# Performance work log

Hardware: AMD Instinct MI355X
Metric: run time of the kernel (lower is better)

Reference implementation:

```python
import jax, jax.numpy as jnp
import numpy as np
import math

B, S, E, H, DFF = 4, 1024, 1024, 16, 4096
HD = E // H
EPS = 1e-8


def setup_inputs() -> dict:
    key = jax.random.key(0)
    ks = jax.random.split(key, 16)
    sc = 0.02
    inp = {
        'x': jax.random.normal(ks[0], (B, S, E), jnp.float32),
        'mask': jax.random.randint(ks[1], (B, S, S), 0, 2, jnp.int32),
        'Wq': jax.random.normal(ks[2], (E, E), jnp.float32) * sc,
        'bq': jnp.zeros((E,), jnp.float32),
        'Wk': jax.random.normal(ks[3], (E, E), jnp.float32) * sc,
        'bk': jnp.zeros((E,), jnp.float32),
        'Wv': jax.random.normal(ks[4], (E, E), jnp.float32) * sc,
        'bv': jnp.zeros((E,), jnp.float32),
        'Wo': jax.random.normal(ks[5], (E, E), jnp.float32) * sc,
        'bo': jnp.zeros((E,), jnp.float32),
        'W1': jax.random.normal(ks[6], (DFF, E), jnp.float32) * sc,
        'b1': jnp.zeros((DFF,), jnp.float32),
        'W2': jax.random.normal(ks[7], (E, DFF), jnp.float32) * sc,
        'b2': jnp.zeros((E,), jnp.float32),
        'g1': jnp.ones((E,), jnp.float32),
        'be1': jnp.zeros((E,), jnp.float32),
        'g2': jnp.ones((E,), jnp.float32),
        'be2': jnp.zeros((E,), jnp.float32),
    }
    return inp


def _layernorm(x, g, b):
    # torch LayerNorm here: (x-mean)/(std+eps), std is unbiased (ddof=1)
    mean = jnp.mean(x, axis=-1, keepdims=True)
    std = jnp.std(x, axis=-1, keepdims=True, ddof=1)
    return g * (x - mean) / (std + EPS) + b


def _gelu(x):
    c = math.sqrt(2.0 / math.pi)
    return 0.5 * x * (1.0 + jnp.tanh(c * (x + 0.044715 * x ** 3)))


def _block(x, mask_f, Wq, bq, Wk, bk, Wv, bv, Wo, bo, W1, b1, W2, b2, g1, be1, g2, be2):
    # --- attention sublayer (pre-norm, residual) ---
    nx = _layernorm(x, g1, be1)
    q = (nx @ Wq.T + bq).reshape(B, S, H, HD).transpose(0, 2, 1, 3)  # [B,H,S,D]
    k = (nx @ Wk.T + bk).reshape(B, S, H, HD).transpose(0, 2, 1, 3)
    v = (nx @ Wv.T + bv).reshape(B, S, H, HD).transpose(0, 2, 1, 3)
    scores = jnp.einsum('bhqd,bhkd->bhqk', q, k) / math.sqrt(HD)
    m = mask_f[:, None, :, :]  # [B,1,S,S]
    scores = jnp.where(m == 0, jnp.float32(-0.01), scores * m)
    p = jax.nn.softmax(scores, axis=-1)
    o = jnp.einsum('bhqk,bhkd->bhqd', p, v)  # [B,H,S,D]
    o = o.transpose(0, 2, 1, 3).reshape(B, S, E)
    x = x + (o @ Wo.T + bo)
    # --- FFN sublayer ---
    nx2 = _layernorm(x, g2, be2)
    ff = _gelu(nx2 @ W1.T + b1) @ W2.T + b2
    return x + ff


def reference(x, mask, Wq, bq, Wk, bk, Wv, bv, Wo, bo, W1, b1, W2, b2, g1, be1, g2, be2):
    mask_f = mask.astype(jnp.float32)
    return _block(x, mask_f, Wq, bq, Wk, bk, Wv, bv, Wo, bo, W1, b1, W2, b2, g1, be1, g2, be2)
```

## Files before the change

kernel.cpp:

```cpp
#include <hip/hip_runtime.h>
#include <math.h>

typedef __attribute__((ext_vector_type(8))) short short8;
typedef __attribute__((ext_vector_type(4))) float f32x4;
typedef __attribute__((ext_vector_type(4))) int   i32x4v;

#define B_   4
#define S_   1024
#define E_   1024
#define H_   16
#define DFF_ 4096

#define HB_MAX 4.0f

__device__ __forceinline__ ushort f2bf(float f){
  unsigned int x = __float_as_uint(f);
  x += 0x7fffu + ((x >> 16) & 1u);
  return (ushort)(x >> 16);
}

__device__ __forceinline__ unsigned int pk_bf16_trunc(float a, float b){
  return __builtin_amdgcn_perm(__float_as_uint(b), __float_as_uint(a), 0x07060302u);
}

__device__ __forceinline__ float gelu_f(float x){
  const float c = 0.7978845608028654f;
  float u = 2.0f * c * (x + 0.044715f * x * x * x);
  return x / (1.0f + __expf(-u));
}

__device__ __forceinline__ void gl2lds16(const void* g, void* l){
  __builtin_amdgcn_global_load_lds(
      (const __attribute__((address_space(1))) void*)g,
      (__attribute__((address_space(3))) void*)l, 16, 0, 0);
}

__device__ __forceinline__ int q8(float x, float s){
  float v = fmaxf(fminf(x * s, 127.f), -127.f);
  return ((int)__builtin_rintf(v)) & 255;
}
__device__ __forceinline__ int pk_i8x4(float a, float b, float c, float d, float s){
  return q8(a,s) | (q8(b,s) << 8) | (q8(c,s) << 16) | (q8(d,s) << 24);
}

__global__ __launch_bounds__(256) void prep_kernel(
    const float* __restrict__ Wq, const float* __restrict__ Wk,
    const float* __restrict__ Wv, const float* __restrict__ Wo,
    const float* __restrict__ W1, const float* __restrict__ W2,
    const float* __restrict__ bq, const float* __restrict__ bk,
    const float* __restrict__ bv, const int* __restrict__ mask,
    unsigned char* __restrict__ bQKV8, float* __restrict__ sQKV,
    unsigned char* __restrict__ bWo8, float* __restrict__ sWo,
    unsigned char* __restrict__ bW18, float* __restrict__ sW1,
    unsigned char* __restrict__ bW28, float* __restrict__ sW2,
    float* __restrict__ cbias, unsigned long long* __restrict__ maskp)
{
  int blk = blockIdx.x, t = threadIdx.x;
  int w = t >> 6, ln = t & 63;

  if (blk < 2048){
    int row = blk * 4 + w;
    const float* src; unsigned char* dst; float* sdst;
    if (row < 1024){      src = Wq + (size_t)row * 1024;
                          dst = bQKV8 + (size_t)row * 1024; sdst = sQKV + row; }
    else if (row < 2048){ src = Wk + (size_t)(row - 1024) * 1024;
                          dst = bQKV8 + (size_t)row * 1024; sdst = sQKV + row; }
    else if (row < 3072){ src = Wv + (size_t)(row - 2048) * 1024;
                          dst = bQKV8 + (size_t)row * 1024; sdst = sQKV + row; }
    else if (row < 4096){ int r = row - 3072; src = Wo + (size_t)r * 1024;
                          dst = bWo8 + (size_t)r * 1024; sdst = sWo + r; }
    else                { int r = row - 4096; src = W1 + (size_t)r * 1024;
                          dst = bW18 + (size_t)r * 1024; sdst = sW1 + r; }
    float4 v[4]; float m = 0.f;
    #pragma unroll
    for (int i = 0; i < 4; i++){
      v[i] = ((const float4*)src)[ln + i * 64];
      m = fmaxf(m, fmaxf(fmaxf(fabsf(v[i].x), fabsf(v[i].y)),
                         fmaxf(fabsf(v[i].z), fabsf(v[i].w))));
    }
    #pragma unroll
    for (int o = 32; o; o >>= 1) m = fmaxf(m, __shfl_xor(m, o));
    float mx = m + 1e-20f, qs = 127.0f / mx;
    #pragma unroll
    for (int i = 0; i < 4; i++)
      ((int*)dst)[ln + i * 64] = pk_i8x4(v[i].x, v[i].y, v[i].z, v[i].w, qs);
    if (ln == 0) *sdst = mx * (1.0f / 127.0f);
    return;
  }
  if (blk < 2304){
    int r = (blk - 2048) * 4 + w;
    const float* src = W2 + (size_t)r * 4096;
    float4 v[16]; float m = 0.f;
    #pragma unroll
    for (int i = 0; i < 16; i++){
      v[i] = ((const float4*)src)[ln + i * 64];
      m = fmaxf(m, fmaxf(fmaxf(fabsf(v[i].x), fabsf(v[i].y)),
                         fmaxf(fabsf(v[i].z), fabsf(v[i].w))));
    }
    #pragma unroll
    for (int o = 32; o; o >>= 1) m = fmaxf(m, __shfl_xor(m, o));
    float mx = m + 1e-20f, qs = 127.0f / mx;
    #pragma unroll
    for (int i = 0; i < 16; i++)
      ((int*)(bW28 + (size_t)r * 4096))[ln + i * 64] =
          pk_i8x4(v[i].x, v[i].y, v[i].z, v[i].w, qs);
    if (ln == 0) sW2[r] = mx * (1.0f / 127.0f);
    return;
  }
  if (blk == 2304){
    #pragma unroll
    for (int r = 0; r < 12; r++){
      int idx = r * 256 + t;
      cbias[idx] = (idx < 1024) ? bq[idx] : (idx < 2048 ? bk[idx - 1024] : bv[idx - 2048]);
    }
    return;
  }
  int wbase = (blk - 2305) * 16 + w * 4;
  #pragma unroll
  for (int j = 0; j < 4; j++){
    int widx = wbase + j;
    int mv = mask[(size_t)widx * 64 + ln];
    unsigned long long bal = __ballot(mv != 0);
    if (ln == 0) maskp[widx] = bal;
  }
}

__global__ __launch_bounds__(256) void ln_i8(const float* __restrict__ x,
    const float* __restrict__ g, const float* __restrict__ be,
    unsigned char* __restrict__ out8, float* __restrict__ sOut){
  int row = blockIdx.x, t = threadIdx.x;
  float4 v = ((const float4*)(x + (size_t)row * E_))[t];
  float s = v.x + v.y + v.z + v.w;
  float q = v.x*v.x + v.y*v.y + v.z*v.z + v.w*v.w;
  #pragma unroll
  for (int o = 32; o; o >>= 1){ s += __shfl_xor(s, o); q += __shfl_xor(q, o); }
  __shared__ float ss[4], sq[4], sm[4];
  int w = t >> 6;
  if ((t & 63) == 0){ ss[w] = s; sq[w] = q; }
  __syncthreads();
  s = ss[0] + ss[1] + ss[2] + ss[3];
  q = sq[0] + sq[1] + sq[2] + sq[3];
  float mean = s * (1.0f / E_);
  float var  = fmaxf((q - (float)E_ * mean * mean) * (1.0f / (E_ - 1)), 0.0f);
  float inv = 1.0f / (sqrtf(var) + 1e-8f);
  float4 gv = ((const float4*)g)[t];
  float4 bv = ((const float4*)be)[t];
  float n0 = gv.x * (v.x - mean) * inv + bv.x;
  float n1 = gv.y * (v.y - mean) * inv + bv.y;
  float n2 = gv.z * (v.z - mean) * inv + bv.z;
  float n3 = gv.w * (v.w - mean) * inv + bv.w;
  float m = fmaxf(fmaxf(fabsf(n0), fabsf(n1)), fmaxf(fabsf(n2), fabsf(n3)));
  #pragma unroll
  for (int o = 32; o; o >>= 1) m = fmaxf(m, __shfl_xor(m, o));
  if ((t & 63) == 0) sm[w] = m;
  __syncthreads();
  float mx = fmaxf(fmaxf(sm[0], sm[1]), fmaxf(sm[2], sm[3])) + 1e-20f;
  float qs = 127.0f / mx;
  ((int*)(out8 + (size_t)row * E_))[t] = pk_i8x4(n0, n1, n2, n3, qs);
  if (t == 0) sOut[row] = mx * (1.0f / 127.0f);
}

__global__ __launch_bounds__(256) void ln2_fuse(const float* __restrict__ x,
    const float* __restrict__ P, const float* __restrict__ bo,
    const float* __restrict__ g, const float* __restrict__ be,
    float* __restrict__ x2, unsigned char* __restrict__ nx28, float* __restrict__ sOut){
  int row = blockIdx.x, t = threadIdx.x;
  size_t idx = (size_t)row * 256 + t;
  float4 v  = ((const float4*)x)[idx];
  float4 p0 = ((const float4*)P)[idx];
  float4 p1 = ((const float4*)P)[idx + 1048576];
  float4 bv0 = ((const float4*)bo)[t];
  v.x += p0.x + p1.x + bv0.x;
  v.y += p0.y + p1.y + bv0.y;
  v.z += p0.z + p1.z + bv0.z;
  v.w += p0.w + p1.w + bv0.w;
  ((float4*)x2)[idx] = v;
  float s = v.x + v.y + v.z + v.w;
  float q = v.x*v.x + v.y*v.y + v.z*v.z + v.w*v.w;
  #pragma unroll
  for (int o = 32; o; o >>= 1){ s += __shfl_xor(s, o); q += __shfl_xor(q, o); }
  __shared__ float ss[4], sq[4], sm[4];
  int w = t >> 6;
  if ((t & 63) == 0){ ss[w] = s; sq[w] = q; }
  __syncthreads();
  s = ss[0] + ss[1] + ss[2] + ss[3];
  q = sq[0] + sq[1] + sq[2] + sq[3];
  float mean = s * (1.0f / E_);
  float var  = fmaxf((q - (float)E_ * mean * mean) * (1.0f / (E_ - 1)), 0.0f);
  float inv = 1.0f / (sqrtf(var) + 1e-8f);
  float4 gv = ((const float4*)g)[t];
  float4 bev = ((const float4*)be)[t];
  float n0 = gv.x * (v.x - mean) * inv + bev.x;
  float n1 = gv.y * (v.y - mean) * inv + bev.y;
  float n2 = gv.z * (v.z - mean) * inv + bev.z;
  float n3 = gv.w * (v.w - mean) * inv + bev.w;
  float m = fmaxf(fmaxf(fabsf(n0), fabsf(n1)), fmaxf(fabsf(n2), fabsf(n3)));
  #pragma unroll
  for (int o = 32; o; o >>= 1) m = fmaxf(m, __shfl_xor(m, o));
  if ((t & 63) == 0) sm[w] = m;
  __syncthreads();
  float mx = fmaxf(fmaxf(sm[0], sm[1]), fmaxf(sm[2], sm[3])) + 1e-20f;
  float qs = 127.0f / mx;
  ((int*)(nx28 + (size_t)row * E_))[t] = pk_i8x4(n0, n1, n2, n3, qs);
  if (t == 0) sOut[row] = mx * (1.0f / 127.0f);
}

__global__ __launch_bounds__(256) void reduce_out(const float* __restrict__ x2,
    const float* __restrict__ P, const float* __restrict__ b2, float* __restrict__ out){
  size_t i = (size_t)blockIdx.x * 256 + threadIdx.x;
  int col4 = i & 255;
  float4 v  = ((const float4*)x2)[i];
  float4 p0 = ((const float4*)P)[i];
  float4 p1 = ((const float4*)P)[i + 1048576];
  float4 bv = ((const float4*)b2)[col4];
  float4 o;
  o.x = v.x + p0.x + p1.x + bv.x;
  o.y = v.y + p0.y + p1.y + bv.y;
  o.z = v.z + p0.z + p1.z + bv.z;
  o.w = v.w + p0.w + p1.w + bv.w;
  ((float4*)out)[i] = o;
}

template<int MODE>
__global__ __launch_bounds__(512) void gemm256_i8(
    const unsigned char* __restrict__ A8, const unsigned char* __restrict__ B8,
    const float* __restrict__ sA, const float* __restrict__ sB,
    const float* __restrict__ bias,
    ushort* __restrict__ Cb, unsigned char* __restrict__ C8, float* __restrict__ Pf,
    int K, int ldc)
{
  __shared__ __align__(16) unsigned char smem[2][2][32768];
  const int t = threadIdx.x, w = t >> 6, ln = t & 63;
  const int quad = ln >> 4, lc = ln & 15;
  const int wm = w >> 2, wn = w & 3;

  const int gx = gridDim.x;
  const int nwg = gx * gridDim.y;
  int f = blockIdx.y * gx + blockIdx.x;
  f = (f & 7) * (nwg >> 3) + (f >> 3);
  const int n0 = (f % gx) * 256;
  const int m0 = (f / gx) * 256;

  int kbeg = 0, nT = K >> 7;
  if (MODE == 2){
    int kh = K >> 1;
    kbeg = blockIdx.z * kh;
    nT = kh >> 7;
    Pf += (size_t)blockIdx.z * (4096 * 1024);
  }

  auto stage_half = [&](const unsigned char* g, unsigned char* l){
    #pragma unroll
    for (int rr = 0; rr < 2; rr++){
      int chunk = rr * 512 + t;
      int row = chunk >> 3;
      int co = ((chunk & 7) ^ (row & 7)) * 16;
      gl2lds16(g + (size_t)row * K + co, l + (size_t)(rr * 512 + (t & 448)) * 16);
    }
  };

  const unsigned char* gA = A8 + (size_t)m0 * K + kbeg;
  const unsigned char* gB = B8 + (size_t)n0 * K + kbeg;

  i32x4v acc[8][4];
  #pragma unroll
  for (int i = 0; i < 8; i++)
    #pragma unroll
    for (int j = 0; j < 4; j++) acc[i][j] = i32x4v{0, 0, 0, 0};

  stage_half(gA,                    &smem[0][0][0]);
  stage_half(gA + (size_t)128 * K,  &smem[0][0][0] + 16384);
  stage_half(gB,                    &smem[0][1][0]);
  stage_half(gB + (size_t)128 * K,  &smem[0][1][0] + 16384);
  asm volatile("s_waitcnt vmcnt(0)" ::: "memory");
  __builtin_amdgcn_s_barrier();
  asm volatile("" ::: "memory");

  for (int tk = 0; tk < nT; tk++){
    const int c = tk & 1;
    const unsigned char* Ab = &smem[c][0][0];
    const unsigned char* Bb = &smem[c][1][0];
    unsigned char* As1 = &smem[c ^ 1][0][0];
    unsigned char* Bs1 = &smem[c ^ 1][1][0];
    const bool pre = (tk + 1 < nT);
    const unsigned char* gAn = gA + (size_t)(tk + 1) * 128;
    const unsigned char* gBn = gB + (size_t)(tk + 1) * 128;

    #pragma unroll
    for (int p = 0; p < 4; p++){
      const int mh = p >> 1, nh = p & 1;
      if (p == 0 && pre){
        stage_half(gAn,                   As1);
        stage_half(gAn + (size_t)128 * K, As1 + 16384);
      }
      if (p == 1 && pre){
        stage_half(gBn,                   Bs1);
        stage_half(gBn + (size_t)128 * K, Bs1 + 16384);
      }
      i32x4v af[4][2], bfr[2][2];
      #pragma unroll
      for (int i = 0; i < 4; i++){
        int row = wm * 128 + (mh * 4 + i) * 16 + lc;
        int sw = row & 7;
        af[i][0] = *(const i32x4v*)(Ab + (size_t)row * 128 + (((0 + quad) ^ sw) * 16));
        af[i][1] = *(const i32x4v*)(Ab + (size_t)row * 128 + (((4 + quad) ^ sw) * 16));
      }
      #pragma unroll
      for (int j = 0; j < 2; j++){
        int row = wn * 64 + (nh * 2 + j) * 16 + lc;
        int sw = row & 7;
        bfr[j][0] = *(const i32x4v*)(Bb + (size_t)row * 128 + (((0 + quad) ^ sw) * 16));
        bfr[j][1] = *(const i32x4v*)(Bb + (size_t)row * 128 + (((4 + quad) ^ sw) * 16));
      }
      __builtin_amdgcn_s_barrier();
      asm volatile("s_waitcnt lgkmcnt(0)" ::: "memory");
      __builtin_amdgcn_s_setprio(1);
      #pragma unroll
      for (int kk2 = 0; kk2 < 2; kk2++)
        #pragma unroll
        for (int i = 0; i < 4; i++)
          #pragma unroll
          for (int j = 0; j < 2; j++)
            acc[mh * 4 + i][nh * 2 + j] = __builtin_amdgcn_mfma_i32_16x16x64_i8(
                af[i][kk2], bfr[j][kk2], acc[mh * 4 + i][nh * 2 + j], 0, 0, 0);
      __builtin_amdgcn_s_setprio(0);
      if (p == 3){
        asm volatile("s_waitcnt vmcnt(0)" ::: "memory");
      }
      __builtin_amdgcn_s_barrier();
      if (p == 3) asm volatile("" ::: "memory");
    }
  }

  if (MODE == 2){
    #pragma unroll
    for (int j = 0; j < 4; j++){
      int col = n0 + wn * 64 + j * 16 + lc;
      float sb = sB[col] * (HB_MAX / 127.0f);
      #pragma unroll
      for (int i = 0; i < 8; i++){
        int row0 = m0 + wm * 128 + i * 16 + quad * 4;
        #pragma unroll
        for (int r = 0; r < 4; r++)
          Pf[(size_t)(row0 + r) * 1024 + col] = (float)acc[i][j][r] * sb;
      }
    }
  } else {
    float sbv[4], bcv[4], scv[4];
    int colv[4];
    #pragma unroll
    for (int j = 0; j < 4; j++){
      int col = n0 + wn * 64 + j * 16 + lc;
      colv[j] = col;
      sbv[j] = sB[col];
      bcv[j] = bias[col];
      scv[j] = (MODE == 0 && col < 1024) ? 0.125f : 1.0f;
    }
    #pragma unroll
    for (int i = 0; i < 8; i++){
      #pragma unroll
      for (int r = 0; r < 4; r++){
        int row = m0 + wm * 128 + i * 16 + quad * 4 + r;
        float sa = sA[row];
        #pragma unroll
        for (int j = 0; j < 4; j++){
          float v = (float)acc[i][j][r] * sa * sbv[j] + bcv[j];
          if (MODE == 0){
            Cb[(size_t)row * ldc + colv[j]] = f2bf(v * scv[j]);
          } else {
            C8[(size_t)row * 4096 + colv[j]] =
                (unsigned char)q8(gelu_f(v), 127.0f / HB_MAX);
          }
        }
      }
    }
  }
}

__global__ __launch_bounds__(256) void vT_kernel(const ushort* __restrict__ QKV,
                                                 ushort* __restrict__ Vt){
  __shared__ ushort tile[64][68];
  int st = blockIdx.x;
  int bh = blockIdx.y;
  int b = bh >> 4, h = bh & 15;
  int t = threadIdx.x;
  #pragma unroll
  for (int it = 0; it < 4; it++){
    int idx = it * 256 + t;
    int r = idx >> 4, c4 = (idx & 15) * 4;
    ushort4 v = *(const ushort4*)(QKV + ((size_t)(b*1024 + st*64 + r)) * 3072 + 2048 + h*64 + c4);
    *(ushort4*)(&tile[r][c4]) = v;
  }
  __syncthreads();
  #pragma unroll
  for (int it = 0; it < 4; it++){
    int idx = it * 256 + t;
    int d = idx >> 4, s4 = (idx & 15) * 4;
    ushort4 o;
    o.x = tile[s4+0][d]; o.y = tile[s4+1][d]; o.z = tile[s4+2][d]; o.w = tile[s4+3][d];
    *(ushort4*)(Vt + ((size_t)bh * 64 + d) * 1024 + st*64 + s4) = o;
  }
}

__global__ __launch_bounds__(256) void attn_kernel(
    const ushort* __restrict__ QKV, const ushort* __restrict__ Vt,
    const unsigned long long* __restrict__ maskp, unsigned char* __restrict__ O8)
{
  __shared__ __align__(16) ushort Ks[2][64 * 64];
  __shared__ __align__(16) ushort Vs[2][64 * 64];
  __shared__ __align__(16) ushort Ps[4][16 * 72];

  const int t = threadIdx.x, w = t >> 6, ln = t & 63;
  const int quad = ln >> 4, lc = ln & 15;
  const int bh = blockIdx.x, b = bh >> 4;
  const int q0 = blockIdx.y * 64;
  const int coff = (bh & 15) * 64;
  const size_t rb = (size_t)b * S_;

  const int myq = q0 + w*16 + lc;
  const ushort* qrow = QKV + (rb + myq) * 3072 + coff;
  short8 qf0 = *(const short8*)(qrow + quad*8);
  short8 qf1 = *(const short8*)(qrow + 32 + quad*8);
  const unsigned long long* mrow = maskp + (rb + myq) * 16;

  auto stage = [&](int kt, int buf){
    int k0 = kt * 64;
    #pragma unroll
    for (int it = 0; it < 2; it++){
      int chunk = it * 256 + t;
      int row = chunk >> 3;
      int co = ((chunk & 7) ^ (row & 7)) * 8;
      gl2lds16(QKV + (rb + k0 + row) * 3072 + 1024 + coff + co,
               Ks[buf] + (size_t)(it*256 + (t & 192)) * 8);
      gl2lds16(Vt + ((size_t)bh * 64 + row) * 1024 + k0 + co,
               Vs[buf] + (size_t)(it*256 + (t & 192)) * 8);
    }
  };

  f32x4 of[4];
  #pragma unroll
  for (int gd = 0; gd < 4; gd++) of[gd] = f32x4{0.f, 0.f, 0.f, 0.f};
  float lsum = 0.0f;
  const float PM = 0.99004983f;

  stage(0, 0);
  for (int kt = 0; kt < 16; kt++){
    int buf = kt & 1;
    unsigned long long m64 = mrow[kt];
    __syncthreads();
    if (kt < 15) stage(kt + 1, buf ^ 1);
    const ushort* ks = Ks[buf];
    const ushort* vs = Vs[buf];

    f32x4 sf[4];
    #pragma unroll
    for (int g = 0; g < 4; g++){
      int krow = g*16 + lc;
      short8 kf0 = *(const short8*)(ks + krow*64 + ((quad       ^ (lc & 7)) * 8));
      short8 kf1 = *(const short8*)(ks + krow*64 + (((4 + quad) ^ (lc & 7)) * 8));
      f32x4 z = f32x4{0.f, 0.f, 0.f, 0.f};
      z = __builtin_amdgcn_mfma_f32_16x16x32_bf16(kf0, qf0, z, 0, 0, 0);
      z = __builtin_amdgcn_mfma_f32_16x16x32_bf16(kf1, qf1, z, 0, 0, 0);
      sf[g] = z;
    }

    #pragma unroll
    for (int g = 0; g < 4; g++){
      unsigned int b4 = (unsigned int)(m64 >> (g*16 + quad*4)) & 0xFu;
      float p0 = (b4 & 1u) ? __expf(sf[g][0]) : PM;
      float p1 = (b4 & 2u) ? __expf(sf[g][1]) : PM;
      float p2 = (b4 & 4u) ? __expf(sf[g][2]) : PM;
      float p3 = (b4 & 8u) ? __expf(sf[g][3]) : PM;
      lsum += p0 + p1 + p2 + p3;
      uint2 pw;
      pw.x = pk_bf16_trunc(p0, p1);
      pw.y = pk_bf16_trunc(p2, p3);
      *(uint2*)(&Ps[w][lc*72 + g*16 + quad*4]) = pw;
    }

    short8 pf0 = *(const short8*)(&Ps[w][lc*72 + quad*8]);
    short8 pf1 = *(const short8*)(&Ps[w][lc*72 + 32 + quad*8]);
    #pragma unroll
    for (int gd = 0; gd < 4; gd++){
      int vrow = gd*16 + lc;
      short8 vf0 = *(const short8*)(vs + vrow*64 + ((quad       ^ (lc & 7)) * 8));
      short8 vf1 = *(const short8*)(vs + vrow*64 + (((4 + quad) ^ (lc & 7)) * 8));
      of[gd] = __builtin_amdgcn_mfma_f32_16x16x32_bf16(vf0, pf0, of[gd], 0, 0, 0);
      of[gd] = __builtin_amdgcn_mfma_f32_16x16x32_bf16(vf1, pf1, of[gd], 0, 0, 0);
    }
  }

  lsum += __shfl_xor(lsum, 16);
  lsum += __shfl_xor(lsum, 32);
  float inv = 1.0f / lsum;

  unsigned char* orow = O8 + (rb + myq) * E_ + coff;
  #pragma unroll
  for (int gd = 0; gd < 4; gd++){
    int pk = pk_i8x4(of[gd][0] * inv, of[gd][1] * inv,
                     of[gd][2] * inv, of[gd][3] * inv, 127.0f / HB_MAX);
    *(int*)(orow + gd*16 + quad*4) = pk;
  }
}

extern "C" void kernel_launch(void* const* d_in, const int* in_sizes, int n_in,
                              void* d_out, int out_size, void* d_ws, size_t ws_size,
                              hipStream_t stream)
{
  const float* x   = (const float*)d_in[0];
  const int*   mask= (const int*)  d_in[1];
  const float* Wq  = (const float*)d_in[2];
  const float* bq  = (const float*)d_in[3];
  const float* Wk  = (const float*)d_in[4];
  const float* bk  = (const float*)d_in[5];
  const float* Wv  = (const float*)d_in[6];
  const float* bv  = (const float*)d_in[7];
  const float* Wo  = (const float*)d_in[8];
  const float* bo  = (const float*)d_in[9];
  const float* W1  = (const float*)d_in[10];
  const float* b1  = (const float*)d_in[11];
  const float* W2  = (const float*)d_in[12];
  const float* b2  = (const float*)d_in[13];
  const float* g1  = (const float*)d_in[14];
  const float* be1 = (const float*)d_in[15];
  const float* g2  = (const float*)d_in[16];
  const float* be2 = (const float*)d_in[17];
  float* out = (float*)d_out;

  char* ws = (char*)d_ws;
  size_t off = 0;
  auto alloc = [&](size_t bytes) -> void* {
    void* p = ws + off; off += (bytes + 255) & ~(size_t)255; return p;
  };
  const size_t MM = 1024 * 1024;
  unsigned char* bQKV8 = (unsigned char*)alloc(3 * MM);
  float* sQKV  = (float*)alloc(3072 * 4);
  unsigned char* bWo8 = (unsigned char*)alloc(MM);
  float* sWo   = (float*)alloc(1024 * 4);
  unsigned char* bW18 = (unsigned char*)alloc(4 * MM);
  float* sW1   = (float*)alloc(4096 * 4);
  unsigned char* bW28 = (unsigned char*)alloc(4 * MM);
  float* sW2   = (float*)alloc(1024 * 4);
  float* cbias = (float*)alloc(3072 * 4);
  unsigned long long* maskp = (unsigned long long*)alloc(65536 * 8);
  unsigned char* nx8  = (unsigned char*)alloc(4 * MM);
  float* sX1   = (float*)alloc(4096 * 4);
  ushort* QKV  = (ushort*)alloc(12 * MM * 2);
  ushort* VtG  = (ushort*)alloc(4 * MM * 2);
  unsigned char* Ob8 = (unsigned char*)alloc(4 * MM);
  float*  x2   = (float*) alloc(4 * MM * 4);
  unsigned char* nx28 = (unsigned char*)alloc(4 * MM);
  float* sX2   = (float*)alloc(4096 * 4);
  unsigned char* hb8  = (unsigned char*)alloc(16 * MM);

  float* Pbuf = (float*)nx8;

  prep_kernel<<<6401, 256, 0, stream>>>(Wq, Wk, Wv, Wo, W1, W2, bq, bk, bv, mask,
                                        bQKV8, sQKV, bWo8, sWo, bW18, sW1, bW28, sW2,
                                        cbias, maskp);

  ln_i8<<<4096, 256, 0, stream>>>(x, g1, be1, nx8, sX1);

  gemm256_i8<0><<<dim3(12, 16), 512, 0, stream>>>(
      nx8, bQKV8, sX1, sQKV, cbias, QKV, nullptr, nullptr, 1024, 3072);

  vT_kernel<<<dim3(16, 64), 256, 0, stream>>>(QKV, VtG);

  attn_kernel<<<dim3(64, 16), 256, 0, stream>>>(QKV, VtG, maskp, Ob8);

  gemm256_i8<2><<<dim3(4, 16, 2), 512, 0, stream>>>(
      Ob8, bWo8, nullptr, sWo, nullptr, nullptr, nullptr, Pbuf, 1024, 1024);

  ln2_fuse<<<4096, 256, 0, stream>>>(x, Pbuf, bo, g2, be2, x2, nx28, sX2);

  gemm256_i8<1><<<dim3(16, 16), 512, 0, stream>>>(
      nx28, bW18, sX2, sW1, b1, nullptr, hb8, nullptr, 1024, 4096);

  gemm256_i8<2><<<dim3(4, 16, 2), 512, 0, stream>>>(
      hb8, bW28, nullptr, sW2, nullptr, nullptr, nullptr, Pbuf, 4096, 1024);

  reduce_out<<<4096, 256, 0, stream>>>(x2, Pbuf, b2, out);
}
```

Measured before the change: 329.8 us.

## Add BN template to int8 GEMM, widen attention blocks, use exp2 softmax

The int8 GEMM gains a BN template parameter so the split-K Wo and W2 projections use 256x128 tiles, giving twice as many workgroups to fill the CUs. The attention kernel moves to 512 threads covering 128 queries per block and prefetches the next mask word. It also relayouts the P scratch to an unpadded contiguous format and raises wave priority around the MFMA sections. Q is now prescaled by log2(e)/8 so softmax can use exp2f instead of expf. The new P layout and changed scale constant must stay consistent with the rest of the code, and smaller GEMM tiles cost some reuse per block.

```diff
diff --git a/kernel.cpp b/kernel.cpp
--- a/kernel.cpp
+++ b/kernel.cpp
@@ -221,7 +221,7 @@
   ((float4*)out)[i] = o;
 }
 
-template<int MODE>
+template<int MODE, int BN>
 __global__ __launch_bounds__(512) void gemm256_i8(
     const unsigned char* __restrict__ A8, const unsigned char* __restrict__ B8,
     const float* __restrict__ sA, const float* __restrict__ sB,
@@ -229,23 +229,28 @@
     ushort* __restrict__ Cb, unsigned char* __restrict__ C8, float* __restrict__ Pf,
     int K, int ldc)
 {
-  __shared__ __align__(16) unsigned char smem[2][2][32768];
+  constexpr int NBW = BN / 64;
+  constexpr int NMW = 8 / NBW;
+  constexpr int WR  = 256 / NMW;
+  constexpr int RF  = WR / 16;
+  constexpr int BSZ = BN * 128;
+  __shared__ __align__(16) unsigned char smem[2][32768 + BSZ];
+
   const int t = threadIdx.x, w = t >> 6, ln = t & 63;
   const int quad = ln >> 4, lc = ln & 15;
-  const int wm = w >> 2, wn = w & 3;
+  const int wm = w / NBW, wn = w % NBW;
 
   const int gx = gridDim.x;
   const int nwg = gx * gridDim.y;
   int f = blockIdx.y * gx + blockIdx.x;
   f = (f & 7) * (nwg >> 3) + (f >> 3);
-  const int n0 = (f % gx) * 256;
+  const int n0 = (f % gx) * BN;
   const int m0 = (f / gx) * 256;
 
   int kbeg = 0, nT = K >> 7;
   if (MODE == 2){
     int kh = K >> 1;
-    kbeg = blockIdx.z * kh;
-    nT = kh >> 7;
+    kbeg = blockIdx.z * kh; nT = kh >> 7;
     Pf += (size_t)blockIdx.z * (4096 * 1024);
   }
 
@@ -258,30 +263,33 @@
       gl2lds16(g + (size_t)row * K + co, l + (size_t)(rr * 512 + (t & 448)) * 16);
     }
   };
+  auto stage_B = [&](const unsigned char* g, unsigned char* l){
+    stage_half(g, l);
+    if (BN == 256) stage_half(g + (size_t)128 * K, l + 16384);
+  };
 
   const unsigned char* gA = A8 + (size_t)m0 * K + kbeg;
   const unsigned char* gB = B8 + (size_t)n0 * K + kbeg;
 
-  i32x4v acc[8][4];
-  #pragma unroll
-  for (int i = 0; i < 8; i++)
+  i32x4v acc[RF][4];
+  #pragma unroll
+  for (int i = 0; i < RF; i++)
     #pragma unroll
     for (int j = 0; j < 4; j++) acc[i][j] = i32x4v{0, 0, 0, 0};
 
-  stage_half(gA,                    &smem[0][0][0]);
-  stage_half(gA + (size_t)128 * K,  &smem[0][0][0] + 16384);
-  stage_half(gB,                    &smem[0][1][0]);
-  stage_half(gB + (size_t)128 * K,  &smem[0][1][0] + 16384);
+  stage_half(gA,                    &smem[0][0]);
+  stage_half(gA + (size_t)128 * K,  &smem[0][0] + 16384);
+  stage_B(gB, &smem[0][0] + 32768);
   asm volatile("s_waitcnt vmcnt(0)" ::: "memory");
   __builtin_amdgcn_s_barrier();
   asm volatile("" ::: "memory");
 
   for (int tk = 0; tk < nT; tk++){
     const int c = tk & 1;
-    const unsigned char* Ab = &smem[c][0][0];
-    const unsigned char* Bb = &smem[c][1][0];
-    unsigned char* As1 = &smem[c ^ 1][0][0];
-    unsigned char* Bs1 = &smem[c ^ 1][1][0];
+    const unsigned char* Ab = &smem[c][0];
+    const unsigned char* Bb = &smem[c][0] + 32768;
+    unsigned char* As1 = &smem[c ^ 1][0];
+    unsigned char* Bs1 = &smem[c ^ 1][0] + 32768;
     const bool pre = (tk + 1 < nT);
     const unsigned char* gAn = gA + (size_t)(tk + 1) * 128;
     const unsigned char* gBn = gB + (size_t)(tk + 1) * 128;
@@ -294,13 +302,12 @@
         stage_half(gAn + (size_t)128 * K, As1 + 16384);
       }
       if (p == 1 && pre){
-        stage_half(gBn,                   Bs1);
-        stage_half(gBn + (size_t)128 * K, Bs1 + 16384);
-      }
-      i32x4v af[4][2], bfr[2][2];
+        stage_B(gBn, Bs1);
+      }
+      i32x4v af[RF/2][2], bfr[2][2];
       #pragma unroll
-      for (int i = 0; i < 4; i++){
-        int row = wm * 128 + (mh * 4 + i) * 16 + lc;
+      for (int i = 0; i < RF/2; i++){
+        int row = wm * WR + (mh * (RF/2) + i) * 16 + lc;
         int sw = row & 7;
         af[i][0] = *(const i32x4v*)(Ab + (size_t)row * 128 + (((0 + quad) ^ sw) * 16));
         af[i][1] = *(const i32x4v*)(Ab + (size_t)row * 128 + (((4 + quad) ^ sw) * 16));
@@ -318,11 +325,11 @@
       #pragma unroll
       for (int kk2 = 0; kk2 < 2; kk2++)
         #pragma unroll
-        for (int i = 0; i < 4; i++)
+        for (int i = 0; i < RF/2; i++)
           #pragma unroll
           for (int j = 0; j < 2; j++)
-            acc[mh * 4 + i][nh * 2 + j] = __builtin_amdgcn_mfma_i32_16x16x64_i8(
-                af[i][kk2], bfr[j][kk2], acc[mh * 4 + i][nh * 2 + j], 0, 0, 0);
+            acc[mh * (RF/2) + i][nh * 2 + j] = __builtin_amdgcn_mfma_i32_16x16x64_i8(
+                af[i][kk2], bfr[j][kk2], acc[mh * (RF/2) + i][nh * 2 + j], 0, 0, 0);
       __builtin_amdgcn_s_setprio(0);
       if (p == 3){
         asm volatile("s_waitcnt vmcnt(0)" ::: "memory");
@@ -338,8 +345,8 @@
       int col = n0 + wn * 64 + j * 16 + lc;
       float sb = sB[col] * (HB_MAX / 127.0f);
       #pragma unroll
-      for (int i = 0; i < 8; i++){
-        int row0 = m0 + wm * 128 + i * 16 + quad * 4;
+      for (int i = 0; i < RF; i++){
+        int row0 = m0 + wm * WR + i * 16 + quad * 4;
         #pragma unroll
         for (int r = 0; r < 4; r++)
           Pf[(size_t)(row0 + r) * 1024 + col] = (float)acc[i][j][r] * sb;
@@ -354,13 +361,13 @@
       colv[j] = col;
       sbv[j] = sB[col];
       bcv[j] = bias[col];
-      scv[j] = (MODE == 0 && col < 1024) ? 0.125f : 1.0f;
-    }
-    #pragma unroll
-    for (int i = 0; i < 8; i++){
+      scv[j] = (MODE == 0 && col < 1024) ? 0.18033688011112042f : 1.0f;
+    }
+    #pragma unroll
+    for (int i = 0; i < RF; i++){
       #pragma unroll
       for (int r = 0; r < 4; r++){
-        int row = m0 + wm * 128 + i * 16 + quad * 4 + r;
+        int row = m0 + wm * WR + i * 16 + quad * 4 + r;
         float sa = sA[row];
         #pragma unroll
         for (int j = 0; j < 4; j++){
@@ -402,18 +409,18 @@
   }
 }
 
-__global__ __launch_bounds__(256) void attn_kernel(
+__global__ __launch_bounds__(512) void attn_kernel(
     const ushort* __restrict__ QKV, const ushort* __restrict__ Vt,
     const unsigned long long* __restrict__ maskp, unsigned char* __restrict__ O8)
 {
   __shared__ __align__(16) ushort Ks[2][64 * 64];
   __shared__ __align__(16) ushort Vs[2][64 * 64];
-  __shared__ __align__(16) ushort Ps[4][16 * 72];
+  __shared__ __align__(16) ushort Ps[8][16 * 64];
 
   const int t = threadIdx.x, w = t >> 6, ln = t & 63;
   const int quad = ln >> 4, lc = ln & 15;
   const int bh = blockIdx.x, b = bh >> 4;
-  const int q0 = blockIdx.y * 64;
+  const int q0 = blockIdx.y * 128;
   const int coff = (bh & 15) * 64;
   const size_t rb = (size_t)b * S_;
 
@@ -425,16 +432,12 @@
 
   auto stage = [&](int kt, int buf){
     int k0 = kt * 64;
-    #pragma unroll
-    for (int it = 0; it < 2; it++){
-      int chunk = it * 256 + t;
-      int row = chunk >> 3;
-      int co = ((chunk & 7) ^ (row & 7)) * 8;
-      gl2lds16(QKV + (rb + k0 + row) * 3072 + 1024 + coff + co,
-               Ks[buf] + (size_t)(it*256 + (t & 192)) * 8);
-      gl2lds16(Vt + ((size_t)bh * 64 + row) * 1024 + k0 + co,
-               Vs[buf] + (size_t)(it*256 + (t & 192)) * 8);
-    }
+    int row = t >> 3;
+    int co = ((t & 7) ^ (row & 7)) * 8;
+    gl2lds16(QKV + (rb + k0 + row) * 3072 + 1024 + coff + co,
+             Ks[buf] + (size_t)(t & 448) * 8);
+    gl2lds16(Vt + ((size_t)bh * 64 + row) * 1024 + k0 + co,
+             Vs[buf] + (size_t)(t & 448) * 8);
   };
 
   f32x4 of[4];
@@ -443,16 +446,20 @@
   float lsum = 0.0f;
   const float PM = 0.99004983f;
 
+  unsigned long long mnext = mrow[0];
   stage(0, 0);
+  char* pw_base = (char*)&Ps[w][0];
   for (int kt = 0; kt < 16; kt++){
     int buf = kt & 1;
-    unsigned long long m64 = mrow[kt];
+    unsigned long long m64 = mnext;
+    if (kt < 15) mnext = mrow[kt + 1];
     __syncthreads();
     if (kt < 15) stage(kt + 1, buf ^ 1);
     const ushort* ks = Ks[buf];
     const ushort* vs = Vs[buf];
 
     f32x4 sf[4];
+    __builtin_amdgcn_s_setprio(1);
     #pragma unroll
     for (int g = 0; g < 4; g++){
       int krow = g*16 + lc;
@@ -463,23 +470,26 @@
       z = __builtin_amdgcn_mfma_f32_16x16x32_bf16(kf1, qf1, z, 0, 0, 0);
       sf[g] = z;
     }
+    __builtin_amdgcn_s_setprio(0);
 
     #pragma unroll
     for (int g = 0; g < 4; g++){
       unsigned int b4 = (unsigned int)(m64 >> (g*16 + quad*4)) & 0xFu;
-      float p0 = (b4 & 1u) ? __expf(sf[g][0]) : PM;
-      float p1 = (b4 & 2u) ? __expf(sf[g][1]) : PM;
-      float p2 = (b4 & 4u) ? __expf(sf[g][2]) : PM;
-      float p3 = (b4 & 8u) ? __expf(sf[g][3]) : PM;
+      float p0 = (b4 & 1u) ? exp2f(sf[g][0]) : PM;
+      float p1 = (b4 & 2u) ? exp2f(sf[g][1]) : PM;
+      float p2 = (b4 & 4u) ? exp2f(sf[g][2]) : PM;
+      float p3 = (b4 & 8u) ? exp2f(sf[g][3]) : PM;
       lsum += p0 + p1 + p2 + p3;
       uint2 pw;
       pw.x = pk_bf16_trunc(p0, p1);
       pw.y = pk_bf16_trunc(p2, p3);
-      *(uint2*)(&Ps[w][lc*72 + g*16 + quad*4]) = pw;
-    }
-
-    short8 pf0 = *(const short8*)(&Ps[w][lc*72 + quad*8]);
-    short8 pf1 = *(const short8*)(&Ps[w][lc*72 + 32 + quad*8]);
+      int pr = 2*g + (quad >> 1);
+      *(uint2*)(pw_base + ((pr*16 + lc) << 4) + ((quad & 1) << 3)) = pw;
+    }
+
+    short8 pf0 = *(const short8*)(pw_base + (ln << 4));
+    short8 pf1 = *(const short8*)(pw_base + 1024 + (ln << 4));
+    __builtin_amdgcn_s_setprio(1);
     #pragma unroll
     for (int gd = 0; gd < 4; gd++){
       int vrow = gd*16 + lc;
@@ -488,6 +498,7 @@
       of[gd] = __builtin_amdgcn_mfma_f32_16x16x32_bf16(vf0, pf0, of[gd], 0, 0, 0);
       of[gd] = __builtin_amdgcn_mfma_f32_16x16x32_bf16(vf1, pf1, of[gd], 0, 0, 0);
     }
+    __builtin_amdgcn_s_setprio(0);
   }
 
   lsum += __shfl_xor(lsum, 16);
@@ -561,22 +572,22 @@
 
   ln_i8<<<4096, 256, 0, stream>>>(x, g1, be1, nx8, sX1);
 
-  gemm256_i8<0><<<dim3(12, 16), 512, 0, stream>>>(
+  gemm256_i8<0, 256><<<dim3(12, 16), 512, 0, stream>>>(
       nx8, bQKV8, sX1, sQKV, cbias, QKV, nullptr, nullptr, 1024, 3072);
 
   vT_kernel<<<dim3(16, 64), 256, 0, stream>>>(QKV, VtG);
 
-  attn_kernel<<<dim3(64, 16), 256, 0, stream>>>(QKV, VtG, maskp, Ob8);
-
-  gemm256_i8<2><<<dim3(4, 16, 2), 512, 0, stream>>>(
+  attn_kernel<<<dim3(64, 8), 512, 0, stream>>>(QKV, VtG, maskp, Ob8);
+
+  gemm256_i8<2, 128><<<dim3(8, 16, 2), 512, 0, stream>>>(
       Ob8, bWo8, nullptr, sWo, nullptr, nullptr, nullptr, Pbuf, 1024, 1024);
 
   ln2_fuse<<<4096, 256, 0, stream>>>(x, Pbuf, bo, g2, be2, x2, nx28, sX2);
 
-  gemm256_i8<1><<<dim3(16, 16), 512, 0, stream>>>(
+  gemm256_i8<1, 256><<<dim3(16, 16), 512, 0, stream>>>(
       nx28, bW18, sX2, sW1, b1, nullptr, hb8, nullptr, 1024, 4096);
 
-  gemm256_i8<2><<<dim3(4, 16, 2), 512, 0, stream>>>(
+  gemm256_i8<2, 128><<<dim3(8, 16, 2), 512, 0, stream>>>(
       hb8, bW28, nullptr, sW2, nullptr, nullptr, nullptr, Pbuf, 4096, 1024);
 
   reduce_out<<<4096, 256, 0, stream>>>(x2, Pbuf, b2, out);
```

Result: faster. 312.2 us (-5.4%).
